# Optimization experiments

Measured on AMD Instinct MI355X. Metric: run time of the kernel, lower is better.

Reference implementation:

```python
import jax, jax.numpy as jnp
import numpy as np

B = 65536
DIM_BODY = 10
DIM_OBJ = 15
NB_OBJ = 3
N_EDGES = 6
D_MP = 128          # dim_mp_output (edge feature dim)
D_IN = DIM_BODY + DIM_OBJ + D_MP  # 153 = dim_phi_critic_input
HID = 256           # hardcoded hidden width of PhiCriticDeepSet
D_PHI = 256         # dim_phi_critic_output / dim_rho_critic_input
D_ACT = 4


def _linear_params(key, fan_in, fan_out):
    # torch nn.Linear default init: U(-1/sqrt(fan_in), 1/sqrt(fan_in))
    lim = 1.0 / np.sqrt(fan_in)
    kw, kb = jax.random.split(key)
    w = jax.random.uniform(kw, (fan_in, fan_out), minval=-lim, maxval=lim, dtype=jnp.float32)
    b = jax.random.uniform(kb, (fan_out,), minval=-lim, maxval=lim, dtype=jnp.float32)
    return w, b


def setup_inputs() -> dict:
    key = jax.random.key(0)
    ks = jax.random.split(key, 11)
    obs = jax.random.normal(ks[0], (B, DIM_BODY + NB_OBJ * DIM_OBJ), dtype=jnp.float32)
    act = jax.random.normal(ks[1], (B, D_ACT), dtype=jnp.float32)
    edge_features = jax.random.normal(ks[2], (B, N_EDGES, D_MP), dtype=jnp.float32)
    # edge -> target object, from self.edge_ids: obj0 <- edges {0,2}, obj1 <- {1,4}, obj2 <- {3,5}
    edges_to = jnp.array([0, 1, 0, 2, 1, 2], dtype=jnp.int32)
    w1, b1 = _linear_params(ks[3], D_IN, HID)   # phi_critic q1 layer1
    w2, b2 = _linear_params(ks[4], HID, D_PHI)  # phi_critic q1 layer2
    w3, b3 = _linear_params(ks[5], D_IN, HID)   # phi_critic q2 layer1
    w4, b4 = _linear_params(ks[6], HID, D_PHI)  # phi_critic q2 layer2
    wr1, br1 = _linear_params(ks[7], D_PHI, 1)  # rho_critic q1
    wr2, br2 = _linear_params(ks[8], D_PHI, 1)  # rho_critic q2
    return dict(obs=obs, act=act, edge_features=edge_features, edges_to=edges_to,
                w1=w1, b1=b1, w2=w2, b2=b2, w3=w3, b3=b3, w4=w4, b4=b4,
                wr1=wr1, br1=br1, wr2=wr2, br2=br2)


def reference(obs, act, edge_features, edges_to,
              w1, b1, w2, b2, w3, b3, w4, b4, wr1, br1, wr2, br2):
    # obs: [B, dim_body + nb_objects*dim_object]; act unused on this branch
    obs_body = obs[:, :DIM_BODY]                                    # [B, 10]
    obs_objects = obs[:, DIM_BODY:].reshape(-1, NB_OBJ, DIM_OBJ)    # [B, 3, 15]
    # per-node max over incoming edge features (torch.max over np.where(edges_to==i))
    ef = jnp.transpose(edge_features, (1, 0, 2))                    # [E, B, D_MP]
    agg = jax.ops.segment_max(ef, edges_to, num_segments=NB_OBJ)    # [3, B, D_MP]
    body_rep = jnp.broadcast_to(obs_body[None], (NB_OBJ,) + obs_body.shape)  # [3, B, 10]
    objs = jnp.transpose(obs_objects, (1, 0, 2))                    # [3, B, 15]
    inp = jnp.concatenate([body_rep, objs, agg], axis=-1)           # [3, B, 153]
    # PhiCriticDeepSet: two parallel 2-layer ReLU MLPs
    x1 = jax.nn.relu(jax.nn.relu(jnp.einsum('nbi,ih->nbh', inp, w1) + b1) @ w2 + b2)
    x2 = jax.nn.relu(jax.nn.relu(jnp.einsum('nbi,ih->nbh', inp, w3) + b3) @ w4 + b4)
    # readout == 'sum' over nodes
    o1 = x1.sum(axis=0)                                             # [B, 256]
    o2 = x2.sum(axis=0)
    # RhoCriticDeepSet: single linear per critic
    q1 = o1 @ wr1 + br1                                             # [B, 1]
    q2 = o2 @ wr2 + br2
    return (q1, q2)
```

## Files before the change

### kernel.cpp

```cpp
#include <hip/hip_runtime.h>
#include <hip/hip_bf16.h>
#include <stdint.h>


#define B_TOT 65536
#define MB 64

typedef __bf16 bf16x8 __attribute__((ext_vector_type(8)));
typedef float f32x4 __attribute__((ext_vector_type(4)));
typedef unsigned short u16x8 __attribute__((ext_vector_type(8)));

#define OFF_W1H 0
#define OFF_W1L 40960
#define OFF_W2H 81920
#define OFF_W2L 147456
#define OFF_W3H 212992
#define OFF_W3L 253952
#define OFF_W4H 294912
#define OFF_W4L 360448

__device__ inline unsigned short f2bf(float f) {
  unsigned int u = __float_as_uint(f);
  u += 0x7fffu + ((u >> 16) & 1u);
  return (unsigned short)(u >> 16);
}
__device__ inline float bf2f(unsigned short h) {
  return __uint_as_float(((unsigned int)h) << 16);
}
__device__ inline void split2(float v, unsigned short& h, unsigned short& l) {
  h = f2bf(v);
  l = f2bf(v - bf2f(h));
}

__global__ void prep_weights(const float* __restrict__ w1, const float* __restrict__ w2,
                             const float* __restrict__ w3, const float* __restrict__ w4,
                             unsigned short* __restrict__ ws) {
  int bid = blockIdx.x;
  int lane = threadIdx.x;
  const float* w; int f, Kreal; unsigned short *oh, *ol;
  if (bid < 80)       { w = w1; f = bid;       Kreal = 153; oh = ws + OFF_W1H; ol = ws + OFF_W1L; }
  else if (bid < 208) { w = w2; f = bid - 80;  Kreal = 256; oh = ws + OFF_W2H; ol = ws + OFF_W2L; }
  else if (bid < 288) { w = w3; f = bid - 208; Kreal = 153; oh = ws + OFF_W3H; ol = ws + OFF_W3L; }
  else                { w = w4; f = bid - 288; Kreal = 256; oh = ws + OFF_W4H; ol = ws + OFF_W4L; }
  int kf = f >> 4, cfg = f & 15;
  int c  = cfg * 16 + (lane & 15);
  int kb = kf * 32 + (lane >> 4) * 8;
  u16x8 H, L;
#pragma unroll
  for (int j = 0; j < 8; ++j) {
    int k = kb + j;
    float v = (k < Kreal) ? w[k * 256 + c] : 0.f;
    unsigned short h, l; split2(v, h, l);
    H[j] = h; L[j] = l;
  }
  size_t idx = ((size_t)f * 64 + lane) * 8;
  *(u16x8*)(oh + idx) = H;
  *(u16x8*)(ol + idx) = L;
}

__device__ inline void zero_acc(f32x4 acc[4][2]) {
#pragma unroll
  for (int rf = 0; rf < 4; ++rf)
#pragma unroll
    for (int cf = 0; cf < 2; ++cf)
      acc[rf][cf] = (f32x4){0.f, 0.f, 0.f, 0.f};
}

template<int KF, int ASTRIDE>
__device__ inline void gemm_phase(const unsigned short* Ah, const unsigned short* Al,
                                  const unsigned short* wH, const unsigned short* wL,
                                  int lane, int wave, f32x4 acc[4][2]) {
  const int arow = lane & 15;
  const int kgr  = (lane >> 4) * 8;
#pragma unroll
  for (int kf = 0; kf < KF; ++kf) {
    bf16x8 ah[4], al[4];
#pragma unroll
    for (int rf = 0; rf < 4; ++rf) {
      ah[rf] = *(const bf16x8*)(Ah + (rf * 16 + arow) * ASTRIDE + kf * 32 + kgr);
      al[rf] = *(const bf16x8*)(Al + (rf * 16 + arow) * ASTRIDE + kf * 32 + kgr);
    }
#pragma unroll
    for (int cf = 0; cf < 2; ++cf) {
      const size_t fidx = ((size_t)(kf * 16 + wave * 2 + cf) * 64 + lane) * 8;
      bf16x8 bh = *(const bf16x8*)(wH + fidx);
      bf16x8 bl = *(const bf16x8*)(wL + fidx);
#pragma unroll
      for (int rf = 0; rf < 4; ++rf) {
        acc[rf][cf] = __builtin_amdgcn_mfma_f32_16x16x32_bf16(ah[rf], bh, acc[rf][cf], 0, 0, 0);
        acc[rf][cf] = __builtin_amdgcn_mfma_f32_16x16x32_bf16(al[rf], bh, acc[rf][cf], 0, 0, 0);
        acc[rf][cf] = __builtin_amdgcn_mfma_f32_16x16x32_bf16(ah[rf], bl, acc[rf][cf], 0, 0, 0);
      }
    }
  }
}

__device__ inline void store_hidden(f32x4 acc[4][2], const float* bias, int lane, int wave,
                                    unsigned short (*Hh)[264], unsigned short (*Hl)[264]) {
  const int col0 = wave * 32 + (lane & 15);
  const int row0 = (lane >> 4) << 2;
#pragma unroll
  for (int rf = 0; rf < 4; ++rf)
#pragma unroll
    for (int cf = 0; cf < 2; ++cf) {
      int col = col0 + cf * 16;
      float bv = bias[col];
#pragma unroll
      for (int i = 0; i < 4; ++i) {
        int row = rf * 16 + row0 + i;
        float h = fmaxf(acc[rf][cf][i] + bv, 0.f);
        unsigned short hh, hl; split2(h, hh, hl);
        Hh[row][col] = hh; Hl[row][col] = hl;
      }
    }
}

__device__ inline void accum_q(f32x4 acc[4][2], const float* bias, const float* wr,
                               int lane, int wave, float qp[4][4]) {
  const int col0 = wave * 32 + (lane & 15);
#pragma unroll
  for (int rf = 0; rf < 4; ++rf)
#pragma unroll
    for (int cf = 0; cf < 2; ++cf) {
      int col = col0 + cf * 16;
      float bv = bias[col];
      float wv = wr[col];
#pragma unroll
      for (int i = 0; i < 4; ++i) {
        float x = fmaxf(acc[rf][cf][i] + bv, 0.f);
        qp[rf][i] += x * wv;
      }
    }
}

__global__ __launch_bounds__(512, 2) void gnn_fused(
    const float* __restrict__ obs, const float* __restrict__ ef, const int* __restrict__ eto,
    const unsigned short* __restrict__ ws,
    const float* __restrict__ b1, const float* __restrict__ b2,
    const float* __restrict__ b3, const float* __restrict__ b4,
    const float* __restrict__ wr1, const float* __restrict__ br1,
    const float* __restrict__ wr2, const float* __restrict__ br2,
    float* __restrict__ out) {
  __shared__ unsigned short A1h[64][168];
  __shared__ unsigned short A1l[64][168];
  __shared__ unsigned short A2h[64][264];
  __shared__ unsigned short A2l[64][264];
  __shared__ float sbias[4][256];
  __shared__ float swr[2][256];
  __shared__ float qbuf[2][8][64];

  const int tid  = threadIdx.x;
  const int lane = tid & 63;
  const int wave = tid >> 6;
  const int b0   = blockIdx.x * MB;

  if (tid < 256) {
    sbias[0][tid] = b1[tid]; sbias[1][tid] = b2[tid];
    sbias[2][tid] = b3[tid]; sbias[3][tid] = b4[tid];
    swr[0][tid]   = wr1[tid]; swr[1][tid]  = wr2[tid];
  }
  int e2s[6];
#pragma unroll
  for (int e = 0; e < 6; ++e) e2s[e] = eto[e];

  float qp1[4][4] = {};
  float qp2[4][4] = {};

  for (int n = 0; n < 3; ++n) {
    for (int idx = tid; idx < 64 * 32; idx += 512) {
      int r = idx >> 5, k = idx & 31;
      if (k < 25) {
        int b = b0 + r;
        float v = (k < 10) ? obs[b * 55 + k] : obs[b * 55 + 10 + n * 15 + (k - 10)];
        unsigned short h, l; split2(v, h, l);
        A1h[r][k] = h; A1l[r][k] = l;
      }
    }
    for (int idx = tid; idx < 64 * 16; idx += 512) {
      int r = idx >> 4, k = 153 + (idx & 15);
      if (k < 168) { A1h[r][k] = 0; A1l[r][k] = 0; }
    }
#pragma unroll
    for (int it = 0; it < 4; ++it) {
      int job = tid + it * 512;
      int r = job >> 5, dq = job & 31;
      size_t b = (size_t)(b0 + r);
      float m0 = -3.0e38f, m1 = m0, m2 = m0, m3 = m0;
#pragma unroll
      for (int e = 0; e < 6; ++e) {
        if (e2s[e] == n) {
          const float4 v = *(const float4*)(ef + (b * 6 + e) * 128 + dq * 4);
          m0 = fmaxf(m0, v.x); m1 = fmaxf(m1, v.y);
          m2 = fmaxf(m2, v.z); m3 = fmaxf(m3, v.w);
        }
      }
      int c = 25 + dq * 4;
      unsigned short h, l;
      split2(m0, h, l); A1h[r][c + 0] = h; A1l[r][c + 0] = l;
      split2(m1, h, l); A1h[r][c + 1] = h; A1l[r][c + 1] = l;
      split2(m2, h, l); A1h[r][c + 2] = h; A1l[r][c + 2] = l;
      split2(m3, h, l); A1h[r][c + 3] = h; A1l[r][c + 3] = l;
    }
    __syncthreads();

    {
      f32x4 acc[4][2]; zero_acc(acc);
      gemm_phase<5, 168>(&A1h[0][0], &A1l[0][0], ws + OFF_W1H, ws + OFF_W1L, lane, wave, acc);
      store_hidden(acc, sbias[0], lane, wave, A2h, A2l);
    }
    __syncthreads();
    {
      f32x4 acc[4][2]; zero_acc(acc);
      gemm_phase<8, 264>(&A2h[0][0], &A2l[0][0], ws + OFF_W2H, ws + OFF_W2L, lane, wave, acc);
      accum_q(acc, sbias[1], swr[0], lane, wave, qp1);
    }
    __syncthreads();
    {
      f32x4 acc[4][2]; zero_acc(acc);
      gemm_phase<5, 168>(&A1h[0][0], &A1l[0][0], ws + OFF_W3H, ws + OFF_W3L, lane, wave, acc);
      store_hidden(acc, sbias[2], lane, wave, A2h, A2l);
    }
    __syncthreads();
    {
      f32x4 acc[4][2]; zero_acc(acc);
      gemm_phase<8, 264>(&A2h[0][0], &A2l[0][0], ws + OFF_W4H, ws + OFF_W4L, lane, wave, acc);
      accum_q(acc, sbias[3], swr[1], lane, wave, qp2);
    }
  }

#pragma unroll
  for (int rf = 0; rf < 4; ++rf)
#pragma unroll
    for (int i = 0; i < 4; ++i) {
      float v1 = qp1[rf][i], v2 = qp2[rf][i];
#pragma unroll
      for (int m = 1; m < 16; m <<= 1) {
        v1 += __shfl_xor(v1, m);
        v2 += __shfl_xor(v2, m);
      }
      if ((lane & 15) == 0) {
        int row = rf * 16 + ((lane >> 4) << 2) + i;
        qbuf[0][wave][row] = v1;
        qbuf[1][wave][row] = v2;
      }
    }
  __syncthreads();
  if (tid < 128) {
    int net = tid >> 6, row = tid & 63;
    float s = 0.f;
#pragma unroll
    for (int w = 0; w < 8; ++w) s += qbuf[net][w][row];
    s += net ? br2[0] : br1[0];
    out[net * B_TOT + b0 + row] = s;
  }
}

extern "C" void kernel_launch(void* const* d_in, const int* in_sizes, int n_in,
                              void* d_out, int out_size, void* d_ws, size_t ws_size,
                              hipStream_t stream) {
  (void)in_sizes; (void)n_in; (void)out_size; (void)ws_size;
  const float* obs = (const float*)d_in[0];
  const float* ef  = (const float*)d_in[2];
  const int*   eto = (const int*)d_in[3];
  const float* w1  = (const float*)d_in[4];  const float* b1  = (const float*)d_in[5];
  const float* w2  = (const float*)d_in[6];  const float* b2  = (const float*)d_in[7];
  const float* w3  = (const float*)d_in[8];  const float* b3  = (const float*)d_in[9];
  const float* w4  = (const float*)d_in[10]; const float* b4  = (const float*)d_in[11];
  const float* wr1 = (const float*)d_in[12]; const float* br1 = (const float*)d_in[13];
  const float* wr2 = (const float*)d_in[14]; const float* br2 = (const float*)d_in[15];
  float* out = (float*)d_out;
  unsigned short* ws = (unsigned short*)d_ws;

  prep_weights<<<416, 64, 0, stream>>>(w1, w2, w3, w4, ws);
  gnn_fused<<<B_TOT / MB, 512, 0, stream>>>(obs, ef, eto, ws,
                                            b1, b2, b3, b4, wr1, br1, wr2, br2, out);
}
```

Measured before the change: 1.047 ms.

## Retile GEMMs to 2x4 wave grid with double-buffered fragment loads

Changes the per-wave output tile from 64 rows x 32 columns to 32 rows x 64 columns using a 2x4 wave grid. This cuts LDS A-fragment reads per wave and raises B-fragment reuse. Fragments for the next k-step are now loaded in registers while MFMAs for the current step run, hiding global and LDS load latency at the cost of more registers. Input loads and output stores also switch to nontemporal hints to reduce cache pollution from streaming data.

```diff
diff --git a/kernel.cpp b/kernel.cpp
--- a/kernel.cpp
+++ b/kernel.cpp
@@ -8,6 +8,7 @@
 
 typedef __bf16 bf16x8 __attribute__((ext_vector_type(8)));
 typedef float f32x4 __attribute__((ext_vector_type(4)));
+typedef float f32x4v __attribute__((ext_vector_type(4)));
 typedef unsigned short u16x8 __attribute__((ext_vector_type(8)));
 
 #define OFF_W1H 0
@@ -58,56 +59,81 @@
   *(u16x8*)(ol + idx) = L;
 }
 
-__device__ inline void zero_acc(f32x4 acc[4][2]) {
-#pragma unroll
-  for (int rf = 0; rf < 4; ++rf)
-#pragma unroll
-    for (int cf = 0; cf < 2; ++cf)
+__device__ __forceinline__ void loadW(bf16x8 (&Wb)[8], const unsigned short* WH,
+                                      const unsigned short* WL, int kf) {
+#pragma unroll
+  for (int cf = 0; cf < 4; ++cf) {
+    Wb[cf * 2 + 0] = *(const bf16x8*)(WH + (size_t)kf * 8192 + cf * 512);
+    Wb[cf * 2 + 1] = *(const bf16x8*)(WL + (size_t)kf * 8192 + cf * 512);
+  }
+}
+template<int AS>
+__device__ __forceinline__ void loadA(bf16x8 (&Ab)[4], const unsigned short* A0h,
+                                      const unsigned short* A0l, int kf) {
+  Ab[0] = *(const bf16x8*)(A0h + kf * 32);
+  Ab[1] = *(const bf16x8*)(A0l + kf * 32);
+  Ab[2] = *(const bf16x8*)(A0h + 16 * AS + kf * 32);
+  Ab[3] = *(const bf16x8*)(A0l + 16 * AS + kf * 32);
+}
+
+template<int KF, int AS>
+__device__ __forceinline__ void gemm2(const unsigned short* __restrict__ Ah,
+                                      const unsigned short* __restrict__ Al,
+                                      const unsigned short* __restrict__ wHb,
+                                      const unsigned short* __restrict__ wLb,
+                                      int lane, int wr, int wc, f32x4 acc[2][4]) {
+  const int r0 = wr * 32 + (lane & 15);
+  const int kg = (lane >> 4) * 8;
+  const unsigned short* A0h = Ah + r0 * AS + kg;
+  const unsigned short* A0l = Al + r0 * AS + kg;
+  const size_t wof = ((size_t)(wc * 4) * 64 + lane) * 8;
+  const unsigned short* WH = wHb + wof;
+  const unsigned short* WL = wLb + wof;
+
+  bf16x8 W[2][8], A[2][4];
+  loadW(W[0], WH, WL, 0);
+  loadA<AS>(A[0], A0h, A0l, 0);
+#pragma unroll
+  for (int kf = 0; kf < KF; ++kf) {
+    const int cu = kf & 1, nx = cu ^ 1;
+    if (kf + 1 < KF) {
+      loadW(W[nx], WH, WL, kf + 1);
+      loadA<AS>(A[nx], A0h, A0l, kf + 1);
+    }
+#pragma unroll
+    for (int cf = 0; cf < 4; ++cf) {
+#pragma unroll
+      for (int rf = 0; rf < 2; ++rf) {
+        acc[rf][cf] = __builtin_amdgcn_mfma_f32_16x16x32_bf16(A[cu][rf*2+0], W[cu][cf*2+0], acc[rf][cf], 0, 0, 0);
+        acc[rf][cf] = __builtin_amdgcn_mfma_f32_16x16x32_bf16(A[cu][rf*2+1], W[cu][cf*2+0], acc[rf][cf], 0, 0, 0);
+        acc[rf][cf] = __builtin_amdgcn_mfma_f32_16x16x32_bf16(A[cu][rf*2+0], W[cu][cf*2+1], acc[rf][cf], 0, 0, 0);
+      }
+    }
+  }
+}
+
+__device__ __forceinline__ void zero_acc(f32x4 acc[2][4]) {
+#pragma unroll
+  for (int rf = 0; rf < 2; ++rf)
+#pragma unroll
+    for (int cf = 0; cf < 4; ++cf)
       acc[rf][cf] = (f32x4){0.f, 0.f, 0.f, 0.f};
 }
 
-template<int KF, int ASTRIDE>
-__device__ inline void gemm_phase(const unsigned short* Ah, const unsigned short* Al,
-                                  const unsigned short* wH, const unsigned short* wL,
-                                  int lane, int wave, f32x4 acc[4][2]) {
-  const int arow = lane & 15;
-  const int kgr  = (lane >> 4) * 8;
-#pragma unroll
-  for (int kf = 0; kf < KF; ++kf) {
-    bf16x8 ah[4], al[4];
-#pragma unroll
-    for (int rf = 0; rf < 4; ++rf) {
-      ah[rf] = *(const bf16x8*)(Ah + (rf * 16 + arow) * ASTRIDE + kf * 32 + kgr);
-      al[rf] = *(const bf16x8*)(Al + (rf * 16 + arow) * ASTRIDE + kf * 32 + kgr);
-    }
-#pragma unroll
-    for (int cf = 0; cf < 2; ++cf) {
-      const size_t fidx = ((size_t)(kf * 16 + wave * 2 + cf) * 64 + lane) * 8;
-      bf16x8 bh = *(const bf16x8*)(wH + fidx);
-      bf16x8 bl = *(const bf16x8*)(wL + fidx);
-#pragma unroll
-      for (int rf = 0; rf < 4; ++rf) {
-        acc[rf][cf] = __builtin_amdgcn_mfma_f32_16x16x32_bf16(ah[rf], bh, acc[rf][cf], 0, 0, 0);
-        acc[rf][cf] = __builtin_amdgcn_mfma_f32_16x16x32_bf16(al[rf], bh, acc[rf][cf], 0, 0, 0);
-        acc[rf][cf] = __builtin_amdgcn_mfma_f32_16x16x32_bf16(ah[rf], bl, acc[rf][cf], 0, 0, 0);
-      }
-    }
-  }
-}
-
-__device__ inline void store_hidden(f32x4 acc[4][2], const float* bias, int lane, int wave,
-                                    unsigned short (*Hh)[264], unsigned short (*Hl)[264]) {
-  const int col0 = wave * 32 + (lane & 15);
-  const int row0 = (lane >> 4) << 2;
-#pragma unroll
-  for (int rf = 0; rf < 4; ++rf)
-#pragma unroll
-    for (int cf = 0; cf < 2; ++cf) {
+__device__ __forceinline__ void store_hidden2(f32x4 acc[2][4], const float* bias,
+                                              int lane, int wr, int wc,
+                                              unsigned short (*Hh)[264], unsigned short (*Hl)[264]) {
+  const int row0 = wr * 32 + ((lane >> 4) << 2);
+  const int col0 = wc * 64 + (lane & 15);
+#pragma unroll
+  for (int rf = 0; rf < 2; ++rf)
+#pragma unroll
+    for (int cf = 0; cf < 4; ++cf) {
       int col = col0 + cf * 16;
       float bv = bias[col];
 #pragma unroll
       for (int i = 0; i < 4; ++i) {
-        int row = rf * 16 + row0 + i;
+        int row = row0 + rf * 16 + i;
         float h = fmaxf(acc[rf][cf][i] + bv, 0.f);
         unsigned short hh, hl; split2(h, hh, hl);
         Hh[row][col] = hh; Hl[row][col] = hl;
@@ -115,16 +141,16 @@
     }
 }
 
-__device__ inline void accum_q(f32x4 acc[4][2], const float* bias, const float* wr,
-                               int lane, int wave, float qp[4][4]) {
-  const int col0 = wave * 32 + (lane & 15);
-#pragma unroll
-  for (int rf = 0; rf < 4; ++rf)
-#pragma unroll
-    for (int cf = 0; cf < 2; ++cf) {
+__device__ __forceinline__ void accum_q2(f32x4 acc[2][4], const float* bias, const float* wrv,
+                                         int lane, int wr, int wc, float qp[2][4]) {
+  const int col0 = wc * 64 + (lane & 15);
+#pragma unroll
+  for (int rf = 0; rf < 2; ++rf)
+#pragma unroll
+    for (int cf = 0; cf < 4; ++cf) {
       int col = col0 + cf * 16;
       float bv = bias[col];
-      float wv = wr[col];
+      float wv = wrv[col];
 #pragma unroll
       for (int i = 0; i < 4; ++i) {
         float x = fmaxf(acc[rf][cf][i] + bv, 0.f);
@@ -147,11 +173,13 @@
   __shared__ unsigned short A2l[64][264];
   __shared__ float sbias[4][256];
   __shared__ float swr[2][256];
-  __shared__ float qbuf[2][8][64];
+  __shared__ float qbuf[2][2][4][32];
 
   const int tid  = threadIdx.x;
   const int lane = tid & 63;
   const int wave = tid >> 6;
+  const int wr   = wave >> 2;
+  const int wc   = wave & 3;
   const int b0   = blockIdx.x * MB;
 
   if (tid < 256) {
@@ -163,15 +191,16 @@
 #pragma unroll
   for (int e = 0; e < 6; ++e) e2s[e] = eto[e];
 
-  float qp1[4][4] = {};
-  float qp2[4][4] = {};
+  float qp1[2][4] = {};
+  float qp2[2][4] = {};
 
   for (int n = 0; n < 3; ++n) {
     for (int idx = tid; idx < 64 * 32; idx += 512) {
       int r = idx >> 5, k = idx & 31;
       if (k < 25) {
         int b = b0 + r;
-        float v = (k < 10) ? obs[b * 55 + k] : obs[b * 55 + 10 + n * 15 + (k - 10)];
+        float v = (k < 10) ? __builtin_nontemporal_load(obs + b * 55 + k)
+                           : __builtin_nontemporal_load(obs + b * 55 + 10 + n * 15 + (k - 10));
         unsigned short h, l; split2(v, h, l);
         A1h[r][k] = h; A1l[r][k] = l;
       }
@@ -189,9 +218,9 @@
 #pragma unroll
       for (int e = 0; e < 6; ++e) {
         if (e2s[e] == n) {
-          const float4 v = *(const float4*)(ef + (b * 6 + e) * 128 + dq * 4);
-          m0 = fmaxf(m0, v.x); m1 = fmaxf(m1, v.y);
-          m2 = fmaxf(m2, v.z); m3 = fmaxf(m3, v.w);
+          const f32x4v v = __builtin_nontemporal_load((const f32x4v*)(ef + (b * 6 + e) * 128 + dq * 4));
+          m0 = fmaxf(m0, v[0]); m1 = fmaxf(m1, v[1]);
+          m2 = fmaxf(m2, v[2]); m3 = fmaxf(m3, v[3]);
         }
       }
       int c = 25 + dq * 4;
@@ -204,32 +233,32 @@
     __syncthreads();
 
     {
-      f32x4 acc[4][2]; zero_acc(acc);
-      gemm_phase<5, 168>(&A1h[0][0], &A1l[0][0], ws + OFF_W1H, ws + OFF_W1L, lane, wave, acc);
-      store_hidden(acc, sbias[0], lane, wave, A2h, A2l);
+      f32x4 acc[2][4]; zero_acc(acc);
+      gemm2<5, 168>(&A1h[0][0], &A1l[0][0], ws + OFF_W1H, ws + OFF_W1L, lane, wr, wc, acc);
+      store_hidden2(acc, sbias[0], lane, wr, wc, A2h, A2l);
     }
     __syncthreads();
     {
-      f32x4 acc[4][2]; zero_acc(acc);
-      gemm_phase<8, 264>(&A2h[0][0], &A2l[0][0], ws + OFF_W2H, ws + OFF_W2L, lane, wave, acc);
-      accum_q(acc, sbias[1], swr[0], lane, wave, qp1);
+      f32x4 acc[2][4]; zero_acc(acc);
+      gemm2<8, 264>(&A2h[0][0], &A2l[0][0], ws + OFF_W2H, ws + OFF_W2L, lane, wr, wc, acc);
+      accum_q2(acc, sbias[1], swr[0], lane, wr, wc, qp1);
     }
     __syncthreads();
     {
-      f32x4 acc[4][2]; zero_acc(acc);
-      gemm_phase<5, 168>(&A1h[0][0], &A1l[0][0], ws + OFF_W3H, ws + OFF_W3L, lane, wave, acc);
-      store_hidden(acc, sbias[2], lane, wave, A2h, A2l);
+      f32x4 acc[2][4]; zero_acc(acc);
+      gemm2<5, 168>(&A1h[0][0], &A1l[0][0], ws + OFF_W3H, ws + OFF_W3L, lane, wr, wc, acc);
+      store_hidden2(acc, sbias[2], lane, wr, wc, A2h, A2l);
     }
     __syncthreads();
     {
-      f32x4 acc[4][2]; zero_acc(acc);
-      gemm_phase<8, 264>(&A2h[0][0], &A2l[0][0], ws + OFF_W4H, ws + OFF_W4L, lane, wave, acc);
-      accum_q(acc, sbias[3], swr[1], lane, wave, qp2);
-    }
-  }
-
-#pragma unroll
-  for (int rf = 0; rf < 4; ++rf)
+      f32x4 acc[2][4]; zero_acc(acc);
+      gemm2<8, 264>(&A2h[0][0], &A2l[0][0], ws + OFF_W4H, ws + OFF_W4L, lane, wr, wc, acc);
+      accum_q2(acc, sbias[3], swr[1], lane, wr, wc, qp2);
+    }
+  }
+
+#pragma unroll
+  for (int rf = 0; rf < 2; ++rf)
 #pragma unroll
     for (int i = 0; i < 4; ++i) {
       float v1 = qp1[rf][i], v2 = qp2[rf][i];
@@ -239,19 +268,19 @@
         v2 += __shfl_xor(v2, m);
       }
       if ((lane & 15) == 0) {
-        int row = rf * 16 + ((lane >> 4) << 2) + i;
-        qbuf[0][wave][row] = v1;
-        qbuf[1][wave][row] = v2;
+        int row32 = rf * 16 + ((lane >> 4) << 2) + i;
+        qbuf[0][wr][wc][row32] = v1;
+        qbuf[1][wr][wc][row32] = v2;
       }
     }
   __syncthreads();
   if (tid < 128) {
-    int net = tid >> 6, row = tid & 63;
+    int net = tid >> 6, r = tid & 63;
     float s = 0.f;
 #pragma unroll
-    for (int w = 0; w < 8; ++w) s += qbuf[net][w][row];
+    for (int w = 0; w < 4; ++w) s += qbuf[net][r >> 5][w][r & 31];
     s += net ? br2[0] : br1[0];
-    out[net * B_TOT + b0 + row] = s;
+    __builtin_nontemporal_store(s, out + net * B_TOT + b0 + r);
   }
 }
 
```

Result: slower. 1.915 ms (+83.0%).
